# Kernel optimization log

Hardware: AMD Instinct MI355X
Metric: run time of the kernel (lower is better)

## Reference

```python
import jax, jax.numpy as jnp
import numpy as np

IN_CH = 512
HID = 512
SCALE = 1.0 / np.sqrt(16.0)  # hard-coded 16**0.5 in source, not sqrt(hidden)


def setup_inputs() -> dict:
    key = jax.random.key(0)
    ks = jax.random.split(key, 9)
    B, T = 8, 2048
    lim = 1.0 / np.sqrt(IN_CH)
    return {
        "q": jax.random.normal(ks[0], (B, T, IN_CH), dtype=jnp.float32),
        "k": jax.random.normal(ks[1], (B, T, IN_CH), dtype=jnp.float32),
        "v": jax.random.normal(ks[2], (B, T, IN_CH), dtype=jnp.float32),
        "Wq": jax.random.uniform(ks[3], (IN_CH, HID), jnp.float32, -lim, lim),
        "bq": jax.random.uniform(ks[4], (HID,), jnp.float32, -lim, lim),
        "Wk": jax.random.uniform(ks[5], (IN_CH, HID), jnp.float32, -lim, lim),
        "bk": jax.random.uniform(ks[6], (HID,), jnp.float32, -lim, lim),
        "Wv": jax.random.uniform(ks[7], (IN_CH, HID), jnp.float32, -lim, lim),
        "bv": jax.random.uniform(ks[8], (HID,), jnp.float32, -lim, lim),
    }


def reference(q, k, v, Wq, bq, Wk, bk, Wv, bv):
    # Linear projections: [B,T,F] @ [F,H] + [H]
    query = jnp.einsum("btf,fh->bth", q, Wq) + bq
    key_p = jnp.einsum("btf,fh->bth", k, Wk) + bk
    value = jnp.einsum("btf,fh->bth", v, Wv) + bv
    # energy: [B,T,T], scaled by fixed 1/sqrt(16)
    energy = jnp.einsum("bth,bsh->bts", query, key_p) * SCALE
    attn = jax.nn.softmax(energy, axis=-1)
    # weighted sum: [B,T,H]
    return jnp.einsum("bts,bsh->bth", attn, value)
```

## Files before the change

### kernel.cpp

```cpp
#include <hip/hip_runtime.h>
#include <stdint.h>

typedef __bf16 bf16;
typedef bf16 bf16x8 __attribute__((ext_vector_type(8)));
typedef float f32x4 __attribute__((ext_vector_type(4)));

#define MFMA(a, b, c) __builtin_amdgcn_mfma_f32_16x16x32_bf16(a, b, c, 0, 0, 0)

#define SCALE_L2E 0.3606737602222409f
#define M0 16.0f

#define WAITVM(N) asm volatile("s_waitcnt vmcnt(" #N ")" ::: "memory")
#define WAITLGKM0 asm volatile("s_waitcnt lgkmcnt(0)" ::: "memory")
#define SBAR __builtin_amdgcn_s_barrier()
#define SCHEDB __builtin_amdgcn_sched_barrier(0)
#define PRIO(x) __builtin_amdgcn_s_setprio(x)

__device__ __forceinline__ void gload_lds16(const void* g, void* l) {
  __builtin_amdgcn_global_load_lds(
      (const __attribute__((address_space(1))) uint32_t*)g,
      (__attribute__((address_space(3))) uint32_t*)l, 16, 0, 0);
}

__global__ void k_wtrans(const float* __restrict__ Wq, const float* __restrict__ Wk,
                         const float* __restrict__ Wv, bf16* __restrict__ Wt) {
  __shared__ float tile[32][33];
  int x = threadIdx.x, y = threadIdx.y;
  int k0 = blockIdx.x * 32, n0 = blockIdx.y * 32, z = blockIdx.z;
  const float* W = (z == 0) ? Wq : (z == 1) ? Wk : Wv;
  for (int j = 0; j < 4; j++)
    tile[y + 8 * j][x] = W[(size_t)(k0 + y + 8 * j) * 512 + n0 + x];
  __syncthreads();
  bf16* o = Wt + (size_t)z * 262144;
  for (int j = 0; j < 4; j++)
    o[(size_t)(n0 + y + 8 * j) * 512 + k0 + x] = (bf16)tile[x][y + 8 * j];
}

__global__ __launch_bounds__(256, 2) void k_proj(
    const float* __restrict__ q, const float* __restrict__ k, const float* __restrict__ v,
    const bf16* __restrict__ Wt, const float* __restrict__ bq, const float* __restrict__ bk,
    const float* __restrict__ bv, bf16* __restrict__ Qp, bf16* __restrict__ Kp,
    bf16* __restrict__ Vtp) {
  int z = blockIdx.z;
  const float* A = (z == 0) ? q : (z == 1) ? k : v;
  const float* bias = (z == 0) ? bq : (z == 1) ? bk : bv;
  const bf16* Bw = Wt + (size_t)z * 262144;

  int m0 = blockIdx.x * 128, n0 = blockIdx.y * 128;
  __shared__ __align__(16) char smem[65536];
  bf16* As = (bf16*)smem;
  bf16* Bs = (bf16*)(smem + 32768);
  bf16* Ts = (bf16*)smem;

  int tid = threadIdx.x;
  int wave = tid >> 6, lane = tid & 63, qr = lane & 15, quad = lane >> 4;
  int wm = (wave >> 1) * 64, wn = (wave & 1) * 64;

  f32x4 acc[4][4];
  for (int mi = 0; mi < 4; mi++)
    for (int ni = 0; ni < 4; ni++) acc[mi][ni] = (f32x4){0.f, 0.f, 0.f, 0.f};

  float4 rxA[4], ryA[4];
  float4 rxB[4], ryB[4];

  auto issueA = [&](int kk, float4 (&rx)[4], float4 (&ry)[4]) {
#pragma unroll
    for (int i = 0; i < 4; i++) {
      int ch = i * 256 + tid, row = ch >> 3, c = ch & 7;
      const float4* src = (const float4*)(A + (size_t)(m0 + row) * 512 + kk + c * 8);
      rx[i] = src[0];
      ry[i] = src[1];
    }
    SCHEDB;
  };

  auto issueB = [&](int kk, int buf) {
#pragma unroll
    for (int i = 0; i < 4; i++) {
      int ch = i * 256 + tid, row = ch >> 3, c = ch & 7, cs = c ^ (row & 7);
      gload_lds16(Bw + (size_t)(n0 + row) * 512 + kk + cs * 8, &Bs[buf * 8192 + ch * 8]);
    }
    SCHEDB;
  };

  auto writeA = [&](int buf, float4 (&rx)[4], float4 (&ry)[4]) {
#pragma unroll
    for (int i = 0; i < 4; i++) {
      int ch = i * 256 + tid, row = ch >> 3, c = ch & 7, cs = c ^ (row & 7);
      bf16x8 t;
      t[0] = (bf16)rx[i].x; t[1] = (bf16)rx[i].y; t[2] = (bf16)rx[i].z; t[3] = (bf16)rx[i].w;
      t[4] = (bf16)ry[i].x; t[5] = (bf16)ry[i].y; t[6] = (bf16)ry[i].z; t[7] = (bf16)ry[i].w;
      *(bf16x8*)&As[buf * 8192 + row * 64 + cs * 8] = t;
    }
  };

  auto compute = [&](int buf) {
    bf16* Ab = &As[buf * 8192];
    bf16* Bb = &Bs[buf * 8192];
#pragma unroll
    for (int h = 0; h < 2; h++) {
      bf16x8 af[4], bfv[4];
#pragma unroll
      for (int mi = 0; mi < 4; mi++) {
        int rr = wm + mi * 16 + qr;
        int cc = (h * 4 + quad) ^ (rr & 7);
        af[mi] = *(bf16x8*)&Ab[rr * 64 + cc * 8];
      }
#pragma unroll
      for (int ni = 0; ni < 4; ni++) {
        int rr = wn + ni * 16 + qr;
        int cc = (h * 4 + quad) ^ (rr & 7);
        bfv[ni] = *(bf16x8*)&Bb[rr * 64 + cc * 8];
      }
#pragma unroll
      for (int mi = 0; mi < 4; mi++)
#pragma unroll
        for (int ni = 0; ni < 4; ni++) acc[mi][ni] = MFMA(af[mi], bfv[ni], acc[mi][ni]);
    }
  };

  issueA(0, rxA, ryA);
  issueA(64, rxB, ryB);
  issueB(0, 0);
  writeA(0, rxA, ryA);
  WAITLGKM0;
  SBAR;

#pragma unroll
  for (int t = 0; t < 8; t += 2) {
    if (t < 6) issueA((t + 2) * 64, rxA, ryA);
    issueB((t + 1) * 64, 1);
    if (t < 6) { WAITVM(12); } else { WAITVM(4); }
    SBAR;
    SCHEDB;
    compute(0);
    writeA(1, rxB, ryB);
    WAITLGKM0;
    SBAR;

    int u = t + 1;
    if (u < 6) issueA((u + 2) * 64, rxB, ryB);
    if (u < 7) issueB((u + 1) * 64, 0);
    if (u < 6) { WAITVM(12); } else { WAITVM(0); }
    SBAR;
    SCHEDB;
    compute(1);
    if (u < 7) writeA(0, rxA, ryA);
    WAITLGKM0;
    SBAR;
  }

  if (z == 2) {
    for (int ni = 0; ni < 4; ni++) {
      int hcol = wn + ni * 16 + qr;
      float bz = bias[n0 + hcol];
      for (int mi = 0; mi < 4; mi++) {
        int tl = wm + mi * 16 + quad * 4;
        bf16 tmp[4];
        for (int r = 0; r < 4; r++) tmp[r] = (bf16)(acc[mi][ni][r] + bz);
        *(uint64_t*)&Ts[hcol * 136 + tl] = *(uint64_t*)tmp;
      }
    }
    __syncthreads();
    int bb = m0 >> 11, t0l = m0 & 2047;
    for (int i = 0; i < 8; i++) {
      int ch = i * 256 + tid;
      int row = ch >> 4, c = ch & 15;
      *(bf16x8*)(Vtp + (size_t)(bb * 512 + n0 + row) * 2048 + t0l + c * 8) =
          *(bf16x8*)&Ts[row * 136 + c * 8];
    }
  } else {
    bf16* C = (z == 0) ? Qp : Kp;
    float sc = (z == 0) ? SCALE_L2E : 1.0f;
    for (int ni = 0; ni < 4; ni++) {
      int col = n0 + wn + ni * 16 + qr;
      float bz = bias[col];
      for (int mi = 0; mi < 4; mi++) {
        int rbase = m0 + wm + mi * 16 + quad * 4;
        for (int r = 0; r < 4; r++)
          C[(size_t)(rbase + r) * 512 + col] = (bf16)((acc[mi][ni][r] + bz) * sc);
      }
    }
  }
}

__global__ __launch_bounds__(512, 1) void k_qk(const bf16* __restrict__ Qp,
                                               const bf16* __restrict__ Kp,
                                               bf16* __restrict__ P,
                                               float* __restrict__ Lpart) {
  __shared__ __align__(16) bf16 S[65536];
  int b = blockIdx.z;
  const bf16* A = Qp + (size_t)b * 2048 * 512;
  const bf16* B = Kp + (size_t)b * 2048 * 512;
  bf16* Pb = P + (size_t)b * 2048 * 2048;
  int m0 = blockIdx.x * 256, n0 = blockIdx.y * 256;
  int tid = threadIdx.x;
  int wave = tid >> 6, lane = tid & 63, qr = lane & 15, quad = lane >> 4;
  int wm = wave >> 2, wn = wave & 3;

  f32x4 acc[8][4];
  for (int mi = 0; mi < 8; mi++)
    for (int ni = 0; ni < 4; ni++) acc[mi][ni] = (f32x4){0.f, 0.f, 0.f, 0.f};

  auto stageAj = [&](int t, int s, int j) {
    int kk = t * 64;
    bf16* As_ = S + s * 16384;
    int ch = j * 512 + tid, row = ch >> 3, c = ch & 7, cs = c ^ (row & 7);
    gload_lds16(A + (size_t)(m0 + row) * 512 + kk + cs * 8, As_ + ch * 8);
  };
  auto stage = [&](int t, int s) {
    int kk = t * 64;
    bf16* Bs_ = S + 32768 + s * 16384;
#pragma unroll
    for (int j = 0; j < 4; j++) {
      int ch = j * 512 + tid, row = ch >> 3, c = ch & 7, cs = c ^ (row & 7);
      gload_lds16(B + (size_t)(n0 + row) * 512 + kk + cs * 8, Bs_ + ch * 8);
    }
    stageAj(t, s, 0);
    stageAj(t, s, 2);
    stageAj(t, s, 1);
    stageAj(t, s, 3);
  };

  stage(0, 0);
  stage(1, 1);

  for (int t = 0; t < 8; t++) {
    int cur = t & 1;
    bf16* As_ = S + cur * 16384;
    bf16* Bs_ = S + 32768 + cur * 16384;

    if (t < 7) { WAITVM(10); } else { WAITVM(2); }
    SBAR;
    bf16x8 aF[4][2], bF[4][2];
#pragma unroll
    for (int mi = 0; mi < 4; mi++)
#pragma unroll
      for (int kk = 0; kk < 2; kk++) {
        int row = wm * 128 + mi * 16 + qr;
        aF[mi][kk] = *(bf16x8*)&As_[row * 64 + ((kk * 4 + quad) ^ (row & 7)) * 8];
      }
#pragma unroll
    for (int ni = 0; ni < 4; ni++)
#pragma unroll
      for (int kk = 0; kk < 2; kk++) {
        int row = wn * 64 + ni * 16 + qr;
        bF[ni][kk] = *(bf16x8*)&Bs_[row * 64 + ((kk * 4 + quad) ^ (row & 7)) * 8];
      }
    WAITLGKM0;
    SCHEDB;
    PRIO(1);
#pragma unroll
    for (int kk = 0; kk < 2; kk++)
#pragma unroll
      for (int mi = 0; mi < 4; mi++)
#pragma unroll
        for (int ni = 0; ni < 4; ni++)
          acc[mi][ni] = MFMA(aF[mi][kk], bF[ni][kk], acc[mi][ni]);
    PRIO(0);

    if (t < 7) { WAITVM(8); } else { WAITVM(0); }
    SBAR;
#pragma unroll
    for (int mi = 0; mi < 4; mi++)
#pragma unroll
      for (int kk = 0; kk < 2; kk++) {
        int row = wm * 128 + 64 + mi * 16 + qr;
        aF[mi][kk] = *(bf16x8*)&As_[row * 64 + ((kk * 4 + quad) ^ (row & 7)) * 8];
      }
    WAITLGKM0;
    SBAR;
    if (t < 6) stage(t + 2, cur);
    SCHEDB;
    PRIO(1);
#pragma unroll
    for (int kk = 0; kk < 2; kk++)
#pragma unroll
      for (int mi = 0; mi < 4; mi++)
#pragma unroll
        for (int ni = 0; ni < 4; ni++)
          acc[4 + mi][ni] = MFMA(aF[mi][kk], bF[ni][kk], acc[4 + mi][ni]);
    PRIO(0);
  }

  int slice = blockIdx.y * 4 + wn;
  float* Lp = Lpart + (size_t)slice * 16384 + b * 2048;
#pragma unroll
  for (int mi = 0; mi < 8; mi++) {
    int rowb = m0 + wm * 128 + mi * 16 + quad * 4;
#pragma unroll
    for (int r = 0; r < 4; r++) {
      float s = 0.f;
      bf16* prow = Pb + (size_t)(rowb + r) * 2048 + n0 + wn * 64 + qr;
#pragma unroll
      for (int ni = 0; ni < 4; ni++) {
        float e = exp2f(acc[mi][ni][r] - M0);
        prow[ni * 16] = (bf16)e;
        s += e;
      }
      s += __shfl_xor(s, 1);
      s += __shfl_xor(s, 2);
      s += __shfl_xor(s, 4);
      s += __shfl_xor(s, 8);
      if (qr == 0) Lp[rowb + r] = s;
    }
  }
}

__global__ __launch_bounds__(512, 1) void k_pv(const bf16* __restrict__ P,
                                               const bf16* __restrict__ Vtp,
                                               const float* __restrict__ Lpart,
                                               float* __restrict__ out) {
  __shared__ __align__(16) bf16 S[49152];
  int b = blockIdx.z;
  const bf16* A = P + (size_t)b * 2048 * 2048;
  const bf16* B = Vtp + (size_t)b * 512 * 2048;
  int m0 = blockIdx.x * 256, n0 = blockIdx.y * 128;
  int tid = threadIdx.x;
  int wave = tid >> 6, lane = tid & 63, qr = lane & 15, quad = lane >> 4;
  int wmi = wave >> 1, wni = wave & 1;

  float linv_own = 0.f;
  if (tid < 256) {
    float s = 0.f;
    for (int j = 0; j < 32; j++) s += Lpart[(size_t)j * 16384 + b * 2048 + m0 + tid];
    linv_own = 1.0f / s;
  }

  f32x4 acc[4][4];
  for (int mi = 0; mi < 4; mi++)
    for (int ni = 0; ni < 4; ni++) acc[mi][ni] = (f32x4){0.f, 0.f, 0.f, 0.f};

  auto stage = [&](int t, int s) {
    int kk = t * 64;
    bf16* As_ = S + s * 16384;
    bf16* Bs_ = S + 32768 + s * 8192;
#pragma unroll
    for (int j = 0; j < 4; j++) {
      int ch = j * 512 + tid, row = ch >> 3, c = ch & 7, cs = c ^ (row & 7);
      gload_lds16(A + (size_t)(m0 + row) * 2048 + kk + cs * 8, As_ + ch * 8);
    }
#pragma unroll
    for (int j = 0; j < 2; j++) {
      int ch = j * 512 + tid, row = ch >> 3, c = ch & 7, cs = c ^ (row & 7);
      gload_lds16(B + (size_t)(n0 + row) * 2048 + kk + cs * 8, Bs_ + ch * 8);
    }
  };

  stage(0, 0);
  stage(1, 1);

  for (int t = 0; t < 32; t++) {
    int cur = t & 1;
    bf16* As_ = S + cur * 16384;
    bf16* Bs_ = S + 32768 + cur * 8192;

    if (t < 31) { WAITVM(6); } else { WAITVM(0); }
    SBAR;
    bf16x8 aF[4][2], bF[4][2];
#pragma unroll
    for (int mi = 0; mi < 4; mi++)
#pragma unroll
      for (int kk = 0; kk < 2; kk++) {
        int row = wmi * 64 + mi * 16 + qr;
        aF[mi][kk] = *(bf16x8*)&As_[row * 64 + ((kk * 4 + quad) ^ (row & 7)) * 8];
      }
#pragma unroll
    for (int ni = 0; ni < 4; ni++)
#pragma unroll
      for (int kk = 0; kk < 2; kk++) {
        int row = wni * 64 + ni * 16 + qr;
        bF[ni][kk] = *(bf16x8*)&Bs_[row * 64 + ((kk * 4 + quad) ^ (row & 7)) * 8];
      }
    WAITLGKM0;
    SBAR;
    if (t < 30) stage(t + 2, cur);
    SCHEDB;
    PRIO(1);
#pragma unroll
    for (int kk = 0; kk < 2; kk++)
#pragma unroll
      for (int mi = 0; mi < 4; mi++)
#pragma unroll
        for (int ni = 0; ni < 4; ni++)
          acc[mi][ni] = MFMA(aF[mi][kk], bF[ni][kk], acc[mi][ni]);
    PRIO(0);
  }

  WAITLGKM0;
  SBAR;
  float* Linv_s = (float*)S;
  if (tid < 256) Linv_s[tid] = linv_own;
  SBAR;

#pragma unroll
  for (int mi = 0; mi < 4; mi++) {
    int rowl = wmi * 64 + mi * 16 + quad * 4;
    float linv[4];
    for (int r = 0; r < 4; r++) linv[r] = Linv_s[rowl + r];
#pragma unroll
    for (int ni = 0; ni < 4; ni++) {
      int col = n0 + wni * 64 + ni * 16 + qr;
      float* og = out + (size_t)(b * 2048 + m0 + rowl) * 512 + col;
      for (int r = 0; r < 4; r++) og[(size_t)r * 512] = acc[mi][ni][r] * linv[r];
    }
  }
}

extern "C" void kernel_launch(void* const* d_in, const int* in_sizes, int n_in,
                              void* d_out, int out_size, void* d_ws, size_t ws_size,
                              hipStream_t stream) {
  (void)in_sizes; (void)n_in; (void)out_size; (void)ws_size;
  const float* q  = (const float*)d_in[0];
  const float* k  = (const float*)d_in[1];
  const float* v  = (const float*)d_in[2];
  const float* Wq = (const float*)d_in[3];
  const float* bq = (const float*)d_in[4];
  const float* Wk = (const float*)d_in[5];
  const float* bk = (const float*)d_in[6];
  const float* Wv = (const float*)d_in[7];
  const float* bv = (const float*)d_in[8];
  float* out = (float*)d_out;

  char* ws = (char*)d_ws;
  bf16* Wt     = (bf16*)(ws);
  bf16* Qp     = (bf16*)(ws + 1572864);
  bf16* Kp     = (bf16*)(ws + 18350080);
  bf16* Vtp    = (bf16*)(ws + 35127296);
  bf16* P      = (bf16*)(ws + 51904512);
  float* Lpart = (float*)(ws + 119013376);

  k_wtrans<<<dim3(16, 16, 3), dim3(32, 8, 1), 0, stream>>>(Wq, Wk, Wv, Wt);
  k_proj<<<dim3(128, 4, 3), 256, 0, stream>>>(q, k, v, Wt, bq, bk, bv, Qp, Kp, Vtp);
  k_qk<<<dim3(8, 8, 8), 512, 0, stream>>>(Qp, Kp, P, Lpart);
  k_pv<<<dim3(8, 4, 8), 512, 0, stream>>>(P, Vtp, Lpart, out);
}
```

Baseline: 272.4 us.

## Single-buffer A tile in projection GEMM and remap attention grids batch-innermost

The projection kernel drops the double-buffered bf16 A tile in LDS and keeps a single A buffer. Converted fp32 data is now written just before each compute step, with an extra barrier after compute. This shrinks LDS from 64KB to 48KB so three blocks can be resident per CU instead of two, at the cost of serialising the A write against compute. Separately, the QK and PV kernels use a flat 1-D grid with batch as the fastest index, which changes block dispatch order and likely spreads batches across XCDs or L2 for better cache locality.

```diff
diff --git a/kernel.cpp b/kernel.cpp
--- a/kernel.cpp
+++ b/kernel.cpp
@@ -36,7 +36,7 @@
     o[(size_t)(n0 + y + 8 * j) * 512 + k0 + x] = (bf16)tile[x][y + 8 * j];
 }
 
-__global__ __launch_bounds__(256, 2) void k_proj(
+__global__ __launch_bounds__(256, 3) void k_proj(
     const float* __restrict__ q, const float* __restrict__ k, const float* __restrict__ v,
     const bf16* __restrict__ Wt, const float* __restrict__ bq, const float* __restrict__ bk,
     const float* __restrict__ bv, bf16* __restrict__ Qp, bf16* __restrict__ Kp,
@@ -47,9 +47,9 @@
   const bf16* Bw = Wt + (size_t)z * 262144;
 
   int m0 = blockIdx.x * 128, n0 = blockIdx.y * 128;
-  __shared__ __align__(16) char smem[65536];
+  __shared__ __align__(16) char smem[49152];
   bf16* As = (bf16*)smem;
-  bf16* Bs = (bf16*)(smem + 32768);
+  bf16* Bs = (bf16*)(smem + 16384);
   bf16* Ts = (bf16*)smem;
 
   int tid = threadIdx.x;
@@ -60,8 +60,8 @@
   for (int mi = 0; mi < 4; mi++)
     for (int ni = 0; ni < 4; ni++) acc[mi][ni] = (f32x4){0.f, 0.f, 0.f, 0.f};
 
-  float4 rxA[4], ryA[4];
-  float4 rxB[4], ryB[4];
+  float4 rxE[4], ryE[4];
+  float4 rxO[4], ryO[4];
 
   auto issueA = [&](int kk, float4 (&rx)[4], float4 (&ry)[4]) {
 #pragma unroll
@@ -83,19 +83,18 @@
     SCHEDB;
   };
 
-  auto writeA = [&](int buf, float4 (&rx)[4], float4 (&ry)[4]) {
+  auto writeA = [&](float4 (&rx)[4], float4 (&ry)[4]) {
 #pragma unroll
     for (int i = 0; i < 4; i++) {
       int ch = i * 256 + tid, row = ch >> 3, c = ch & 7, cs = c ^ (row & 7);
       bf16x8 t;
       t[0] = (bf16)rx[i].x; t[1] = (bf16)rx[i].y; t[2] = (bf16)rx[i].z; t[3] = (bf16)rx[i].w;
       t[4] = (bf16)ry[i].x; t[5] = (bf16)ry[i].y; t[6] = (bf16)ry[i].z; t[7] = (bf16)ry[i].w;
-      *(bf16x8*)&As[buf * 8192 + row * 64 + cs * 8] = t;
+      *(bf16x8*)&As[row * 64 + cs * 8] = t;
     }
   };
 
   auto compute = [&](int buf) {
-    bf16* Ab = &As[buf * 8192];
     bf16* Bb = &Bs[buf * 8192];
 #pragma unroll
     for (int h = 0; h < 2; h++) {
@@ -104,7 +103,7 @@
       for (int mi = 0; mi < 4; mi++) {
         int rr = wm + mi * 16 + qr;
         int cc = (h * 4 + quad) ^ (rr & 7);
-        af[mi] = *(bf16x8*)&Ab[rr * 64 + cc * 8];
+        af[mi] = *(bf16x8*)&As[rr * 64 + cc * 8];
       }
 #pragma unroll
       for (int ni = 0; ni < 4; ni++) {
@@ -119,34 +118,31 @@
     }
   };
 
-  issueA(0, rxA, ryA);
-  issueA(64, rxB, ryB);
+  issueA(0, rxE, ryE);
   issueB(0, 0);
-  writeA(0, rxA, ryA);
-  WAITLGKM0;
-  SBAR;
+  issueA(64, rxO, ryO);
 
 #pragma unroll
   for (int t = 0; t < 8; t += 2) {
-    if (t < 6) issueA((t + 2) * 64, rxA, ryA);
+    writeA(rxE, ryE);
     issueB((t + 1) * 64, 1);
-    if (t < 6) { WAITVM(12); } else { WAITVM(4); }
+    if (t < 6) issueA((t + 2) * 64, rxE, ryE);
+    if (t < 6) { WAITVM(20); } else { WAITVM(12); }
+    WAITLGKM0;
     SBAR;
     SCHEDB;
     compute(0);
-    writeA(1, rxB, ryB);
+    SBAR;
+
+    int u = t + 1;
+    writeA(rxO, ryO);
+    if (u < 7) issueB((u + 1) * 64, 0);
+    if (u < 6) issueA((u + 2) * 64, rxO, ryO);
+    if (u < 6) { WAITVM(20); } else if (u < 7) { WAITVM(12); } else { WAITVM(0); }
     WAITLGKM0;
     SBAR;
-
-    int u = t + 1;
-    if (u < 6) issueA((u + 2) * 64, rxB, ryB);
-    if (u < 7) issueB((u + 1) * 64, 0);
-    if (u < 6) { WAITVM(12); } else { WAITVM(0); }
-    SBAR;
     SCHEDB;
     compute(1);
-    if (u < 7) writeA(0, rxA, ryA);
-    WAITLGKM0;
     SBAR;
   }
 
@@ -189,11 +185,13 @@
                                                bf16* __restrict__ P,
                                                float* __restrict__ Lpart) {
   __shared__ __align__(16) bf16 S[65536];
-  int b = blockIdx.z;
+  int id = blockIdx.x;
+  int b = id & 7, j = id >> 3;
+  int mx = j & 7, ny = j >> 3;
   const bf16* A = Qp + (size_t)b * 2048 * 512;
   const bf16* B = Kp + (size_t)b * 2048 * 512;
   bf16* Pb = P + (size_t)b * 2048 * 2048;
-  int m0 = blockIdx.x * 256, n0 = blockIdx.y * 256;
+  int m0 = mx * 256, n0 = ny * 256;
   int tid = threadIdx.x;
   int wave = tid >> 6, lane = tid & 63, qr = lane & 15, quad = lane >> 4;
   int wm = wave >> 2, wn = wave & 3;
@@ -202,18 +200,18 @@
   for (int mi = 0; mi < 8; mi++)
     for (int ni = 0; ni < 4; ni++) acc[mi][ni] = (f32x4){0.f, 0.f, 0.f, 0.f};
 
-  auto stageAj = [&](int t, int s, int j) {
+  auto stageAj = [&](int t, int s, int jj) {
     int kk = t * 64;
     bf16* As_ = S + s * 16384;
-    int ch = j * 512 + tid, row = ch >> 3, c = ch & 7, cs = c ^ (row & 7);
+    int ch = jj * 512 + tid, row = ch >> 3, c = ch & 7, cs = c ^ (row & 7);
     gload_lds16(A + (size_t)(m0 + row) * 512 + kk + cs * 8, As_ + ch * 8);
   };
   auto stage = [&](int t, int s) {
     int kk = t * 64;
     bf16* Bs_ = S + 32768 + s * 16384;
 #pragma unroll
-    for (int j = 0; j < 4; j++) {
-      int ch = j * 512 + tid, row = ch >> 3, c = ch & 7, cs = c ^ (row & 7);
+    for (int jj = 0; jj < 4; jj++) {
+      int ch = jj * 512 + tid, row = ch >> 3, c = ch & 7, cs = c ^ (row & 7);
       gload_lds16(B + (size_t)(n0 + row) * 512 + kk + cs * 8, Bs_ + ch * 8);
     }
     stageAj(t, s, 0);
@@ -283,7 +281,7 @@
     PRIO(0);
   }
 
-  int slice = blockIdx.y * 4 + wn;
+  int slice = ny * 4 + wn;
   float* Lp = Lpart + (size_t)slice * 16384 + b * 2048;
 #pragma unroll
   for (int mi = 0; mi < 8; mi++) {
@@ -312,10 +310,12 @@
                                                const float* __restrict__ Lpart,
                                                float* __restrict__ out) {
   __shared__ __align__(16) bf16 S[49152];
-  int b = blockIdx.z;
+  int id = blockIdx.x;
+  int b = id & 7, j = id >> 3;
+  int mx = j & 7, ny = j >> 3;
   const bf16* A = P + (size_t)b * 2048 * 2048;
   const bf16* B = Vtp + (size_t)b * 512 * 2048;
-  int m0 = blockIdx.x * 256, n0 = blockIdx.y * 128;
+  int m0 = mx * 256, n0 = ny * 128;
   int tid = threadIdx.x;
   int wave = tid >> 6, lane = tid & 63, qr = lane & 15, quad = lane >> 4;
   int wmi = wave >> 1, wni = wave & 1;
@@ -323,7 +323,7 @@
   float linv_own = 0.f;
   if (tid < 256) {
     float s = 0.f;
-    for (int j = 0; j < 32; j++) s += Lpart[(size_t)j * 16384 + b * 2048 + m0 + tid];
+    for (int jj = 0; jj < 32; jj++) s += Lpart[(size_t)jj * 16384 + b * 2048 + m0 + tid];
     linv_own = 1.0f / s;
   }
 
@@ -336,13 +336,13 @@
     bf16* As_ = S + s * 16384;
     bf16* Bs_ = S + 32768 + s * 8192;
 #pragma unroll
-    for (int j = 0; j < 4; j++) {
-      int ch = j * 512 + tid, row = ch >> 3, c = ch & 7, cs = c ^ (row & 7);
+    for (int jj = 0; jj < 4; jj++) {
+      int ch = jj * 512 + tid, row = ch >> 3, c = ch & 7, cs = c ^ (row & 7);
       gload_lds16(A + (size_t)(m0 + row) * 2048 + kk + cs * 8, As_ + ch * 8);
     }
 #pragma unroll
-    for (int j = 0; j < 2; j++) {
-      int ch = j * 512 + tid, row = ch >> 3, c = ch & 7, cs = c ^ (row & 7);
+    for (int jj = 0; jj < 2; jj++) {
+      int ch = jj * 512 + tid, row = ch >> 3, c = ch & 7, cs = c ^ (row & 7);
       gload_lds16(B + (size_t)(n0 + row) * 2048 + kk + cs * 8, Bs_ + ch * 8);
     }
   };
@@ -432,6 +432,6 @@
 
   k_wtrans<<<dim3(16, 16, 3), dim3(32, 8, 1), 0, stream>>>(Wq, Wk, Wv, Wt);
   k_proj<<<dim3(128, 4, 3), 256, 0, stream>>>(q, k, v, Wt, bq, bk, bv, Qp, Kp, Vtp);
-  k_qk<<<dim3(8, 8, 8), 512, 0, stream>>>(Qp, Kp, P, Lpart);
-  k_pv<<<dim3(8, 4, 8), 512, 0, stream>>>(P, Vtp, Lpart, out);
-}
+  k_qk<<<512, 512, 0, stream>>>(Qp, Kp, P, Lpart);
+  k_pv<<<256, 512, 0, stream>>>(P, Vtp, Lpart, out);
+}
```

New measurement: 261.6 us. -4.0%, faster.
